# Optimization experiments

Hardware: AMD Instinct MI355X
Metric: run time of the kernel (lower is better)

Reference implementation:

```python
import jax, jax.numpy as jnp
import numpy as np


def _gcn_layer(x, W, b, src, dst, norm, n_nodes):
    # x: [N, Fin]; transform first (PyG GCNConv): h = x @ W
    h = x @ W  # [N, Fout]
    # gather-scale-scatter: out[d] += norm_e * h[s] over edges (incl. self loops)
    msgs = h[src] * norm[:, None]  # [E+N, Fout]
    agg = jax.ops.segment_sum(msgs, dst, num_segments=n_nodes)
    return agg + b


def setup_inputs() -> dict:
    key = jax.random.key(0)
    k1, k2, k3, k4 = jax.random.split(key, 4)
    N, E, F_IN, HID, OUT = 50000, 800000, 128, 256, 128
    x = jax.random.normal(k1, (N, F_IN), dtype=jnp.float32)
    edge_index = jax.random.randint(k2, (2, E), 0, N, dtype=jnp.int64)
    W1 = jax.random.normal(k3, (F_IN, HID), dtype=jnp.float32) / np.sqrt(F_IN)
    b1 = jnp.zeros((HID,), dtype=jnp.float32)
    W2 = jax.random.normal(k4, (HID, OUT), dtype=jnp.float32) / np.sqrt(HID)
    b2 = jnp.zeros((OUT,), dtype=jnp.float32)
    return {"x": x, "edge_index": edge_index, "W1": W1, "b1": b1, "W2": W2, "b2": b2}


def reference(x, edge_index, W1, b1, W2, b2):
    N = x.shape[0]
    # GCN normalization with self loops: A_hat = D^-1/2 (A + I) D^-1/2
    self_loops = jnp.arange(N, dtype=edge_index.dtype)
    src = jnp.concatenate([edge_index[0], self_loops])
    dst = jnp.concatenate([edge_index[1], self_loops])
    deg = jax.ops.segment_sum(jnp.ones_like(dst, dtype=x.dtype), dst, num_segments=N)
    dinv = jnp.where(deg > 0, jax.lax.rsqrt(deg), 0.0)
    norm = dinv[src] * dinv[dst]  # [E+N]
    h = _gcn_layer(x, W1, b1, src, dst, norm, N)
    h = jax.nn.relu(h)  # dropout is identity in eval mode
    out = _gcn_layer(h, W2, b2, src, dst, norm, N)
    return out  # unsupervised mode returns raw embeddings [N, 128]
```

## Files before the change

### kernel.cpp

```cpp
#include <hip/hip_runtime.h>
#include <hip/hip_bf16.h>


static constexpr int N_NODES = 50000;
static constexpr int N_EDGES = 800000;
static constexpr int F_IN = 128;
static constexpr int HID  = 256;
static constexpr int F_OUT = 128;
static constexpr int NREP = 16;

typedef __attribute__((ext_vector_type(8))) short short8;
typedef __attribute__((ext_vector_type(4))) float f32x4;

__device__ __forceinline__ unsigned short f2bf(float f) {
    union { float f; unsigned u; } x; x.f = f;
    unsigned r = x.u + 0x7FFF + ((x.u >> 16) & 1);
    return (unsigned short)(r >> 16);
}
__device__ __forceinline__ float bf2f(unsigned short h) {
    union { unsigned u; float f; } x; x.u = ((unsigned)h) << 16;
    return x.f;
}

__global__ void deg_wt_kernel(const int* __restrict__ dst, int* __restrict__ deg,
                              int* __restrict__ pos, int E,
                              const float* __restrict__ W1, unsigned short* __restrict__ w1t,
                              const float* __restrict__ W2, unsigned short* __restrict__ w2t,
                              int EB, int NB1) {
    const int b = blockIdx.x;
    if (b < EB) {
        int i = b * 256 + threadIdx.x;
        if (i < E) pos[i] = atomicAdd(&deg[dst[i]], 1);
    } else if (b < EB + NB1) {
        int t = (b - EB) * 256 + threadIdx.x;
        if (t < F_IN * HID) {
            int n = t / F_IN, k = t - n * F_IN;
            unsigned short v = f2bf(W1[(size_t)k * HID + n]);
#pragma unroll
            for (int r = 0; r < NREP; r++) w1t[(size_t)r * F_IN * HID + t] = v;
        }
    } else {
        int t = (b - EB - NB1) * 256 + threadIdx.x;
        if (t < HID * F_OUT) {
            int n = t / HID, k = t - n * HID;
            unsigned short v = f2bf(W2[(size_t)k * F_OUT + n]);
#pragma unroll
            for (int r = 0; r < NREP; r++) w2t[(size_t)r * HID * F_OUT + t] = v;
        }
    }
}

__global__ __launch_bounds__(256) void scan_reduce_dinv(const int* __restrict__ deg,
                                                        int* __restrict__ bsums,
                                                        float* __restrict__ dinv, int N) {
    int i = blockIdx.x * 256 + threadIdx.x;
    int v = (i < N) ? deg[i] : 0;
    if (i < N) dinv[i] = rsqrtf((float)(v + 1));
#pragma unroll
    for (int ofs = 32; ofs > 0; ofs >>= 1) v += __shfl_down(v, ofs);
    __shared__ int ws[4];
    if ((threadIdx.x & 63) == 0) ws[threadIdx.x >> 6] = v;
    __syncthreads();
    if (threadIdx.x == 0) bsums[blockIdx.x] = ws[0] + ws[1] + ws[2] + ws[3];
}

__global__ __launch_bounds__(256) void scan_final_scalex(const int* __restrict__ deg,
                                                         const int* __restrict__ bsums,
                                                         int* __restrict__ off, int N, int nb,
                                                         const float* __restrict__ x,
                                                         const float* __restrict__ dinv,
                                                         unsigned short* __restrict__ xs) {
    const int tid = threadIdx.x;
    if ((int)blockIdx.x >= nb) {
        int i = (blockIdx.x - nb) * 256 + tid;
        if (i < N_NODES * F_IN / 8) {
            float dv = dinv[i >> 4];
            float4 v0 = ((const float4*)x)[i * 2];
            float4 v1 = ((const float4*)x)[i * 2 + 1];
            short8 o;
            o[0] = (short)f2bf(v0.x * dv); o[1] = (short)f2bf(v0.y * dv);
            o[2] = (short)f2bf(v0.z * dv); o[3] = (short)f2bf(v0.w * dv);
            o[4] = (short)f2bf(v1.x * dv); o[5] = (short)f2bf(v1.y * dv);
            o[6] = (short)f2bf(v1.z * dv); o[7] = (short)f2bf(v1.w * dv);
            *(short8*)(xs + (size_t)i * 8) = o;
        }
        return;
    }
    __shared__ int bs[256];
    __shared__ int s[256];
    bs[tid] = (tid < nb) ? bsums[tid] : 0;
    const int i = blockIdx.x * 256 + tid;
    int v = (i < N) ? deg[i] : 0;
    s[tid] = v;
    __syncthreads();
    for (int ofs = 1; ofs < 256; ofs <<= 1) {
        int tb = (tid >= ofs) ? bs[tid - ofs] : 0;
        int tv = (tid >= ofs) ? s[tid - ofs] : 0;
        __syncthreads();
        bs[tid] += tb;
        s[tid] += tv;
        __syncthreads();
    }
    int bbase = (blockIdx.x == 0) ? 0 : bs[blockIdx.x - 1];
    int excl = (tid == 0) ? 0 : s[tid - 1];
    if (i <= N) off[i] = bbase + excl;
}

__global__ void scatter_kernel(const int* __restrict__ src, const int* __restrict__ dst,
                               const int* __restrict__ pos, const int* __restrict__ off,
                               int* __restrict__ csr, int E) {
    int i = blockIdx.x * blockDim.x + threadIdx.x;
    if (i < E) csr[off[dst[i]] + pos[i]] = src[i];
}

template <int MODE>
__global__ __launch_bounds__(256) void agg_bf16(const unsigned short* __restrict__ hs,
                                                const int* __restrict__ off,
                                                const int* __restrict__ csr,
                                                const float* __restrict__ dinv,
                                                const float* __restrict__ bias,
                                                void* __restrict__ outp, int N) {
    const int wid = threadIdx.x >> 6;
    const int n = blockIdx.x * 4 + wid;
    if (n >= N) return;
    const int lane = threadIdx.x & 63;
    const int lane16 = lane & 15;
    const int slot = lane >> 4;

    float va[8], vb[8], vc[8], vd[8];
#pragma unroll
    for (int j = 0; j < 8; j++) { va[j] = 0.f; vb[j] = 0.f; vc[j] = 0.f; vd[j] = 0.f; }

    if (slot == 0) {
        short8 s = *(const short8*)(hs + (size_t)n * 128 + lane16 * 8);
#pragma unroll
        for (int j = 0; j < 8; j++) va[j] = bf2f((unsigned short)s[j]);
    }

    const int e0 = off[n];
    const int e1 = off[n + 1];
    int e = e0 + slot;
    for (; e + 12 < e1; e += 16) {
        int s0 = csr[e];
        int s1 = csr[e + 4];
        int s2 = csr[e + 8];
        int s3 = csr[e + 12];
        short8 v0 = *(const short8*)(hs + (size_t)s0 * 128 + lane16 * 8);
        short8 v1 = *(const short8*)(hs + (size_t)s1 * 128 + lane16 * 8);
        short8 v2 = *(const short8*)(hs + (size_t)s2 * 128 + lane16 * 8);
        short8 v3 = *(const short8*)(hs + (size_t)s3 * 128 + lane16 * 8);
#pragma unroll
        for (int j = 0; j < 8; j++) va[j] += bf2f((unsigned short)v0[j]);
#pragma unroll
        for (int j = 0; j < 8; j++) vb[j] += bf2f((unsigned short)v1[j]);
#pragma unroll
        for (int j = 0; j < 8; j++) vc[j] += bf2f((unsigned short)v2[j]);
#pragma unroll
        for (int j = 0; j < 8; j++) vd[j] += bf2f((unsigned short)v3[j]);
    }
    for (; e < e1; e += 4) {
        int s0 = csr[e];
        short8 v0 = *(const short8*)(hs + (size_t)s0 * 128 + lane16 * 8);
#pragma unroll
        for (int j = 0; j < 8; j++) va[j] += bf2f((unsigned short)v0[j]);
    }
#pragma unroll
    for (int j = 0; j < 8; j++) va[j] += vb[j] + vc[j] + vd[j];

#pragma unroll
    for (int j = 0; j < 8; j++) va[j] += __shfl_down(va[j], 32);
#pragma unroll
    for (int j = 0; j < 8; j++) va[j] += __shfl_down(va[j], 16);

    if (lane < 16) {
        float dv = dinv[n];
        if (MODE == 0) {
            short8 o;
#pragma unroll
            for (int j = 0; j < 8; j++) o[j] = (short)f2bf(va[j] * dv);
            *(short8*)((unsigned short*)outp + (size_t)n * 128 + lane * 8) = o;
        } else {
            float* op = (float*)outp + (size_t)n * 128 + lane * 8;
            float4 o0, o1;
            o0.x = va[0] * dv + bias[lane * 8 + 0];
            o0.y = va[1] * dv + bias[lane * 8 + 1];
            o0.z = va[2] * dv + bias[lane * 8 + 2];
            o0.w = va[3] * dv + bias[lane * 8 + 3];
            o1.x = va[4] * dv + bias[lane * 8 + 4];
            o1.y = va[5] * dv + bias[lane * 8 + 5];
            o1.z = va[6] * dv + bias[lane * 8 + 6];
            o1.w = va[7] * dv + bias[lane * 8 + 7];
            ((float4*)op)[0] = o0;
            ((float4*)op)[1] = o1;
        }
    }
}

__global__ __launch_bounds__(512, 2) void gemm1(const unsigned short* __restrict__ Y,
                                                const unsigned short* __restrict__ w1t,
                                                const float* __restrict__ b1,
                                                unsigned short* __restrict__ h2, int M) {
    __shared__ unsigned short w1l[F_IN * HID];

    const int tid = threadIdx.x;
    const int wid = tid >> 6;
    const int lane = tid & 63;
    const int an = lane & 15;
    const int q = lane >> 4;
    const int rep = blockIdx.x & (NREP - 1);

    {
        const unsigned short* w1r = w1t + (size_t)rep * F_IN * HID;
        for (int i = tid; i < 4096; i += 512) {
            const int cw = i >> 9;
            const int t  = (i >> 8) & 1;
            const int c  = (i >> 6) & 3;
            const int l  = i & 63;
            const int col = cw * 32 + t * 16 + (l & 15);
            const int off = col * F_IN + (l >> 4) * 8 + c * 32;
            *(short8*)(w1l + (size_t)i * 8) = *(const short8*)(w1r + off);
        }
    }
    float bvs[16];
#pragma unroll
    for (int t = 0; t < 16; t++) bvs[t] = b1[t * 16 + an];
    __syncthreads();

    const int m0 = blockIdx.x * 128 + wid * 16;
    int row = m0 + an;
    if (row >= M) row = M - 1;
    short8 a[4];
    {
        const unsigned short* yp = Y + (size_t)row * F_IN + q * 8;
#pragma unroll
        for (int c = 0; c < 4; c++) a[c] = *(const short8*)(yp + c * 32);
    }
    const int mb = m0 + q * 4;
#pragma unroll
    for (int tt = 0; tt < 16; tt++) {
        f32x4 acc = {0.f, 0.f, 0.f, 0.f};
#pragma unroll
        for (int c = 0; c < 4; c++) {
            const short8 b = *(const short8*)(w1l +
                              ((size_t)(((tt >> 1) * 8 + (tt & 1) * 4 + c) * 64 + lane)) * 8);
            acc = __builtin_amdgcn_mfma_f32_16x16x32_bf16(a[c], b, acc, 0, 0, 0);
        }
        const int col = tt * 16 + an;
#pragma unroll
        for (int rr = 0; rr < 4; rr++) {
            const int m = mb + rr;
            if (m < M) h2[(size_t)m * HID + col] = f2bf(fmaxf(acc[rr] + bvs[tt], 0.f));
        }
    }
}

__global__ __launch_bounds__(512, 2) void gemm2(const unsigned short* __restrict__ h2,
                                                const unsigned short* __restrict__ w2t,
                                                const float* __restrict__ dinv,
                                                unsigned short* __restrict__ hs2, int M) {
    __shared__ unsigned short w2l[HID * F_OUT];

    const int tid = threadIdx.x;
    const int wid = tid >> 6;
    const int lane = tid & 63;
    const int an = lane & 15;
    const int q = lane >> 4;
    const int rep = blockIdx.x & (NREP - 1);

    {
        const unsigned short* w2r = w2t + (size_t)rep * HID * F_OUT;
        for (int i = tid; i < 4096; i += 512) {
            const int cw = i >> 9;
            const int c  = (i >> 6) & 7;
            const int l  = i & 63;
            const int colB = cw * 16 + (l & 15);
            const int off = colB * HID + (l >> 4) * 8 + c * 32;
            *(short8*)(w2l + (size_t)i * 8) = *(const short8*)(w2r + off);
        }
    }
    __syncthreads();

    const int m0 = blockIdx.x * 128 + wid * 16;
    int row = m0 + an;
    if (row >= M) row = M - 1;
    short8 a[8];
    {
        const unsigned short* hp = h2 + (size_t)row * HID + q * 8;
#pragma unroll
        for (int c = 0; c < 8; c++) a[c] = *(const short8*)(hp + c * 32);
    }
    const int mb = m0 + q * 4;
    float dv[4];
#pragma unroll
    for (int rr = 0; rr < 4; rr++) dv[rr] = (mb + rr < M) ? dinv[mb + rr] : 0.f;
#pragma unroll
    for (int tt = 0; tt < 8; tt++) {
        f32x4 acc = {0.f, 0.f, 0.f, 0.f};
#pragma unroll
        for (int c = 0; c < 8; c++) {
            const short8 b = *(const short8*)(w2l + ((size_t)((tt * 8 + c) * 64 + lane)) * 8);
            acc = __builtin_amdgcn_mfma_f32_16x16x32_bf16(a[c], b, acc, 0, 0, 0);
        }
        const int col = tt * 16 + an;
#pragma unroll
        for (int rr = 0; rr < 4; rr++) {
            const int m = mb + rr;
            if (m < M) hs2[(size_t)m * F_OUT + col] = f2bf(acc[rr] * dv[rr]);
        }
    }
}

extern "C" void kernel_launch(void* const* d_in, const int* in_sizes, int n_in,
                              void* d_out, int out_size, void* d_ws, size_t ws_size,
                              hipStream_t stream) {
    const float* x  = (const float*)d_in[0];
    const int*   ei = (const int*)d_in[1];
    const float* W1 = (const float*)d_in[2];
    const float* b1 = (const float*)d_in[3];
    const float* W2 = (const float*)d_in[4];
    const float* b2 = (const float*)d_in[5];

    const int N = N_NODES;
    const int E = N_EDGES;
    const int* srcp = ei;
    const int* dstp = ei + E;

    char* base = (char*)d_ws;
    size_t o = 0;
    auto alloc = [&](size_t bytes) {
        void* p = base + o;
        o = (o + bytes + 255) & ~(size_t)255;
        return p;
    };
    int*            deg  = (int*)alloc((size_t)N * 4);
    int*            offs = (int*)alloc((size_t)(N + 1) * 4);
    float*          dinv = (float*)alloc((size_t)N * 4);
    int*            bsum = (int*)alloc(256 * 4);
    int*            pos  = (int*)alloc((size_t)E * 4);
    int*            csr  = (int*)alloc((size_t)E * 4);
    unsigned short* xs   = (unsigned short*)alloc((size_t)N * F_IN * 2);
    unsigned short* Y    = (unsigned short*)alloc((size_t)N * F_IN * 2);
    unsigned short* h2   = (unsigned short*)alloc((size_t)N * HID * 2);
    unsigned short* w1t  = (unsigned short*)alloc((size_t)NREP * F_IN * HID * 2);
    unsigned short* w2t  = (unsigned short*)alloc((size_t)NREP * HID * F_OUT * 2);
    unsigned short* hs2  = xs;

    hipMemsetAsync(deg, 0, (size_t)N * 4, stream);

    const int NB  = (N + 256) / 256;
    const int NBX = (N * F_IN / 8 + 255) / 256;
    const int EB  = (E + 255) / 256;
    const int NB1 = (F_IN * HID + 255) / 256;
    const int NB2 = (HID * F_OUT + 255) / 256;
    const int GB  = (N + 127) / 128;

    deg_wt_kernel<<<EB + NB1 + NB2, 256, 0, stream>>>(dstp, deg, pos, E, W1, w1t, W2, w2t, EB, NB1);
    scan_reduce_dinv<<<NB, 256, 0, stream>>>(deg, bsum, dinv, N);
    scan_final_scalex<<<NB + NBX, 256, 0, stream>>>(deg, bsum, offs, N, NB, x, dinv, xs);
    scatter_kernel<<<EB, 256, 0, stream>>>(srcp, dstp, pos, offs, csr, E);

    agg_bf16<0><<<(N + 3) / 4, 256, 0, stream>>>(xs, offs, csr, dinv, nullptr, Y, N);
    gemm1<<<GB, 512, 0, stream>>>(Y, w1t, b1, h2, N);
    gemm2<<<GB, 512, 0, stream>>>(h2, w2t, dinv, hs2, N);
    agg_bf16<1><<<(N + 3) / 4, 256, 0, stream>>>(hs2, offs, csr, dinv, b2, d_out, N);
}
```

Measured before the change: 246.3 us.

## Pad CSR rows to multiples of 16 with zero-row sentinel and byte offsets

Each node's CSR row is rounded up to a multiple of 16 entries. Padding slots point to an extra all-zero feature row at index N, which lets the aggregation loop drop its scalar tail loop and always run full 4-way unrolled iterations. CSR entries now hold precomputed byte offsets (src<<8), removing the per-gather index multiply. The scatter kernel gets extra blocks to fill the padding, and the scans work on padded degrees. The cost is extra loads of the zero row (likely cache-resident) and a larger CSR array.

```diff
diff --git a/kernel.cpp b/kernel.cpp
--- a/kernel.cpp
+++ b/kernel.cpp
@@ -54,8 +54,9 @@
                                                         int* __restrict__ bsums,
                                                         float* __restrict__ dinv, int N) {
     int i = blockIdx.x * 256 + threadIdx.x;
-    int v = (i < N) ? deg[i] : 0;
-    if (i < N) dinv[i] = rsqrtf((float)(v + 1));
+    int d = (i < N) ? deg[i] : 0;
+    if (i < N) dinv[i] = rsqrtf((float)(d + 1));
+    int v = (i < N) ? ((d + 15) & ~15) : 0;
 #pragma unroll
     for (int ofs = 32; ofs > 0; ofs >>= 1) v += __shfl_down(v, ofs);
     __shared__ int ws[4];
@@ -90,7 +91,7 @@
     __shared__ int s[256];
     bs[tid] = (tid < nb) ? bsums[tid] : 0;
     const int i = blockIdx.x * 256 + tid;
-    int v = (i < N) ? deg[i] : 0;
+    int v = (i < N) ? ((deg[i] + 15) & ~15) : 0;
     s[tid] = v;
     __syncthreads();
     for (int ofs = 1; ofs < 256; ofs <<= 1) {
@@ -108,9 +109,19 @@
 
 __global__ void scatter_kernel(const int* __restrict__ src, const int* __restrict__ dst,
                                const int* __restrict__ pos, const int* __restrict__ off,
-                               int* __restrict__ csr, int E) {
-    int i = blockIdx.x * blockDim.x + threadIdx.x;
-    if (i < E) csr[off[dst[i]] + pos[i]] = src[i];
+                               const int* __restrict__ deg, int* __restrict__ csr,
+                               int E, int N, int EB) {
+    const int b = blockIdx.x;
+    if (b < EB) {
+        int i = b * 256 + threadIdx.x;
+        if (i < E) csr[off[dst[i]] + pos[i]] = src[i] << 8;
+    } else {
+        int n = (b - EB) * 256 + threadIdx.x;
+        if (n < N) {
+            const int zoff = N << 8;
+            for (int e = off[n] + deg[n]; e < off[n + 1]; e++) csr[e] = zoff;
+        }
+    }
 }
 
 template <int MODE>
@@ -126,29 +137,29 @@
     const int lane = threadIdx.x & 63;
     const int lane16 = lane & 15;
     const int slot = lane >> 4;
+    const char* hsl = (const char*)hs + lane16 * 16;
 
     float va[8], vb[8], vc[8], vd[8];
 #pragma unroll
     for (int j = 0; j < 8; j++) { va[j] = 0.f; vb[j] = 0.f; vc[j] = 0.f; vd[j] = 0.f; }
 
     if (slot == 0) {
-        short8 s = *(const short8*)(hs + (size_t)n * 128 + lane16 * 8);
+        short8 s = *(const short8*)(hsl + ((size_t)n << 8));
 #pragma unroll
         for (int j = 0; j < 8; j++) va[j] = bf2f((unsigned short)s[j]);
     }
 
     const int e0 = off[n];
     const int e1 = off[n + 1];
-    int e = e0 + slot;
-    for (; e + 12 < e1; e += 16) {
-        int s0 = csr[e];
-        int s1 = csr[e + 4];
-        int s2 = csr[e + 8];
-        int s3 = csr[e + 12];
-        short8 v0 = *(const short8*)(hs + (size_t)s0 * 128 + lane16 * 8);
-        short8 v1 = *(const short8*)(hs + (size_t)s1 * 128 + lane16 * 8);
-        short8 v2 = *(const short8*)(hs + (size_t)s2 * 128 + lane16 * 8);
-        short8 v3 = *(const short8*)(hs + (size_t)s3 * 128 + lane16 * 8);
+    for (int e = e0 + slot; e < e1; e += 16) {
+        int o0 = csr[e];
+        int o1 = csr[e + 4];
+        int o2 = csr[e + 8];
+        int o3 = csr[e + 12];
+        short8 v0 = *(const short8*)(hsl + (unsigned)o0);
+        short8 v1 = *(const short8*)(hsl + (unsigned)o1);
+        short8 v2 = *(const short8*)(hsl + (unsigned)o2);
+        short8 v3 = *(const short8*)(hsl + (unsigned)o3);
 #pragma unroll
         for (int j = 0; j < 8; j++) va[j] += bf2f((unsigned short)v0[j]);
 #pragma unroll
@@ -157,12 +168,6 @@
         for (int j = 0; j < 8; j++) vc[j] += bf2f((unsigned short)v2[j]);
 #pragma unroll
         for (int j = 0; j < 8; j++) vd[j] += bf2f((unsigned short)v3[j]);
-    }
-    for (; e < e1; e += 4) {
-        int s0 = csr[e];
-        short8 v0 = *(const short8*)(hs + (size_t)s0 * 128 + lane16 * 8);
-#pragma unroll
-        for (int j = 0; j < 8; j++) va[j] += bf2f((unsigned short)v0[j]);
     }
 #pragma unroll
     for (int j = 0; j < 8; j++) va[j] += vb[j] + vc[j] + vd[j];
@@ -337,8 +342,8 @@
     float*          dinv = (float*)alloc((size_t)N * 4);
     int*            bsum = (int*)alloc(256 * 4);
     int*            pos  = (int*)alloc((size_t)E * 4);
-    int*            csr  = (int*)alloc((size_t)E * 4);
-    unsigned short* xs   = (unsigned short*)alloc((size_t)N * F_IN * 2);
+    int*            csr  = (int*)alloc(((size_t)E + 16 * (N + 1)) * 4);
+    unsigned short* xs   = (unsigned short*)alloc((size_t)(N + 1) * F_IN * 2);
     unsigned short* Y    = (unsigned short*)alloc((size_t)N * F_IN * 2);
     unsigned short* h2   = (unsigned short*)alloc((size_t)N * HID * 2);
     unsigned short* w1t  = (unsigned short*)alloc((size_t)NREP * F_IN * HID * 2);
@@ -346,9 +351,11 @@
     unsigned short* hs2  = xs;
 
     hipMemsetAsync(deg, 0, (size_t)N * 4, stream);
+    hipMemsetAsync(xs + (size_t)N * F_IN, 0, F_IN * 2, stream);
 
     const int NB  = (N + 256) / 256;
     const int NBX = (N * F_IN / 8 + 255) / 256;
+    const int NBn = (N + 255) / 256;
     const int EB  = (E + 255) / 256;
     const int NB1 = (F_IN * HID + 255) / 256;
     const int NB2 = (HID * F_OUT + 255) / 256;
@@ -357,7 +364,7 @@
     deg_wt_kernel<<<EB + NB1 + NB2, 256, 0, stream>>>(dstp, deg, pos, E, W1, w1t, W2, w2t, EB, NB1);
     scan_reduce_dinv<<<NB, 256, 0, stream>>>(deg, bsum, dinv, N);
     scan_final_scalex<<<NB + NBX, 256, 0, stream>>>(deg, bsum, offs, N, NB, x, dinv, xs);
-    scatter_kernel<<<EB, 256, 0, stream>>>(srcp, dstp, pos, offs, csr, E);
+    scatter_kernel<<<EB + NBn, 256, 0, stream>>>(srcp, dstp, pos, offs, deg, csr, E, N, EB);
 
     agg_bf16<0><<<(N + 3) / 4, 256, 0, stream>>>(xs, offs, csr, dinv, nullptr, Y, N);
     gemm1<<<GB, 512, 0, stream>>>(Y, w1t, b1, h2, N);
```

After: 235.8 us. 1.04x faster.
